# Kernel tuning notes

Hardware: AMD Instinct MI355X
Metric: run time of the kernel (lower is better)

The kernel has to match this reference:

```python
import jax, jax.numpy as jnp
import numpy as np

INPUT_DIM = 128
NUM_CLASSES = 10
MAX_DEPTH = 8
HID = 16            # effective_transform_output_dim
TEMP = 1.0
EFF_IN = INPUT_DIM + 2          # root features + parent score + grandparent score
N_INTERNAL = 2 ** MAX_DEPTH - 1  # 255, level-order stacked
N_LEAVES = 2 ** MAX_DEPTH        # 256
BATCH = 32768


def setup_inputs() -> dict:
    key = jax.random.key(0)
    ks = jax.random.split(key, 6)
    x = jax.random.normal(ks[0], (BATCH, INPUT_DIM), jnp.float32)
    path_prob = jnp.ones((BATCH, 1), jnp.float32)
    W1 = jax.random.normal(ks[1], (N_INTERNAL, EFF_IN, HID), jnp.float32) * (1.0 / np.sqrt(EFF_IN))
    b1 = jax.random.normal(ks[2], (N_INTERNAL, HID), jnp.float32) * 0.01
    w2 = jax.random.normal(ks[3], (N_INTERNAL, HID), jnp.float32) * (1.0 / np.sqrt(HID))
    b2 = jax.random.normal(ks[4], (N_INTERNAL,), jnp.float32) * 0.01
    leaf_logits = jax.random.normal(ks[5], (N_LEAVES, NUM_CLASSES), jnp.float32)
    return {"x": x, "path_prob": path_prob, "W1": W1, "b1": b1,
            "w2": w2, "b2": b2, "leaf_logits": leaf_logits}


def reference(x, path_prob, W1, b1, w2, b2, leaf_logits):
    """Depth-batched soft binary tree: all 2^d nodes at depth d are processed
    as one batched GEMM instead of the original sequential recursion."""
    B = x.shape[0]
    pp = path_prob                              # [B, n_nodes_at_depth]
    parent = jnp.zeros((B, 1), x.dtype)         # parent decision scores (0 => unused at depth 0)
    grandp = jnp.zeros((B, 1), x.dtype)         # grandparent scores (0 => unused at depth 0,1)
    for d in range(MAX_DEPTH):
        lo, hi = 2 ** d - 1, 2 ** (d + 1) - 1   # level-order slice of this depth's nodes
        W1d = W1[lo:hi]                          # [N, EFF_IN, HID]
        # concat([x, parent, grandparent]) @ W1d without materializing the concat
        h = jnp.einsum('be,neh->bnh', x, W1d[:, :INPUT_DIM, :])
        h = h + parent[:, :, None] * W1d[None, :, INPUT_DIM, :]
        h = h + grandp[:, :, None] * W1d[None, :, INPUT_DIM + 1, :]
        t = jax.nn.relu(h + b1[lo:hi][None])                       # [B, N, HID]
        score = jnp.einsum('bnh,nh->bn', t, w2[lo:hi]) + b2[lo:hi][None]  # [B, N]
        p = jax.nn.sigmoid(score / TEMP)
        n = pp.shape[1]
        # children: left gets p, right gets 1-p; level-order interleave
        pp = jnp.stack([pp * p, pp * (1.0 - p)], axis=-1).reshape(B, 2 * n)
        grandp = jnp.repeat(parent, 2, axis=1)   # child's grandparent = node's parent
        parent = jnp.repeat(score, 2, axis=1)    # child's parent_out = this node's raw score
    # leaves: sum_n path_prob[:, n] * output_logits[n]
    return jnp.einsum('bn,nc->bc', pp, leaf_logits)
```

## Files before the change

kernel.cpp:

```cpp
#include <hip/hip_runtime.h>
#include <math.h>

namespace {

typedef __attribute__((ext_vector_type(8))) __fp16 f16x8;
typedef __attribute__((ext_vector_type(4))) float f32x4;

constexpr int IN_DIM = 128;
constexpr int EFF    = 130 * 16;
constexpr int NODES  = 255;
constexpr int TS     = 64;
constexpr int BLOCK  = 256;
constexpr int NC     = 10;

__global__ __launch_bounds__(256) void prep_w1(const float* __restrict__ W1,
                                               f16x8* __restrict__ wfrag) {
    __shared__ float xs[IN_DIM * 16];
    const int n = blockIdx.x, tid = threadIdx.x;
    const float4* src = (const float4*)(W1 + (size_t)n * EFF);
    ((float4*)xs)[tid]       = src[tid];
    ((float4*)xs)[tid + 256] = src[tid + 256];
    __syncthreads();
    const int l = tid & 63, t = tid >> 6;
    const int k0 = t * 32 + (l >> 4) * 8, hid = l & 15;
    f16x8 hv;
    #pragma unroll
    for (int j = 0; j < 8; ++j)
        hv[j] = (__fp16)xs[(k0 + j) * 16 + hid];
    wfrag[(n * 4 + t) * 64 + l] = hv;
}

__device__ __forceinline__ void loadW(const f16x8* __restrict__ wfrag, int n, int l,
                                      f16x8 (&w)[4]) {
    const f16x8* wp = wfrag + (size_t)n * 256 + l;
    #pragma unroll
    for (int t = 0; t < 4; ++t) w[t] = wp[t * 64];
}

__device__ __forceinline__ void mfma16(const f16x8 (&w)[4], const f16x8 (&xh)[4][4],
                                       f32x4 (&acc)[4]) {
    #pragma unroll
    for (int t = 0; t < 4; ++t)
        #pragma unroll
        for (int mt = 0; mt < 4; ++mt)
            acc[mt] = __builtin_amdgcn_mfma_f32_16x16x32_f16(w[t], xh[t][mt], acc[mt], 0, 0, 0);
}

__device__ __forceinline__ float epilogue_score(
    const f32x4 (&acc)[4], const float4& w2q, const float4& wpq, const float4& wgq,
    const float (&par)[4], const float (&gp)[4], float b2v, int quad)
{
    float score01[4];
    #pragma unroll
    for (int mt = 0; mt < 4; ++mt) {
        float ts = 0.0f;
        #pragma unroll
        for (int r = 0; r < 4; ++r) {
            const float wpr = (r == 0) ? wpq.x : (r == 1) ? wpq.y : (r == 2) ? wpq.z : wpq.w;
            const float wgr = (r == 0) ? wgq.x : (r == 1) ? wgq.y : (r == 2) ? wgq.z : wgq.w;
            const float w2r = (r == 0) ? w2q.x : (r == 1) ? w2q.y : (r == 2) ? w2q.z : w2q.w;
            const float h = fmaf(par[mt], wpr, fmaf(gp[mt], wgr, acc[mt][r]));
            ts = fmaf(fmaxf(h, 0.0f), w2r, ts);
        }
        ts += __shfl_xor(ts, 16);
        ts += __shfl_xor(ts, 32);
        score01[mt] = ts;
    }
    const float sa = (quad & 1) ? score01[1] : score01[0];
    const float sb = (quad & 1) ? score01[3] : score01[2];
    return ((quad & 2) ? sb : sa) + b2v;
}

__global__ __launch_bounds__(BLOCK) __attribute__((amdgpu_waves_per_eu(2, 2)))
void tree_mfma(
    const float* __restrict__ x, const float* __restrict__ path_prob,
    const float* __restrict__ W1, const float* __restrict__ b1,
    const float* __restrict__ w2, const float* __restrict__ b2,
    const float* __restrict__ leaf_logits,
    const f16x8* __restrict__ wfrag,
    float* __restrict__ out)
{
    __shared__ float pp[128][TS];
    __shared__ float scbuf[127][TS];

    const int tid  = threadIdx.x;
    const int wv   = tid >> 6, l = tid & 63;
    const int quad = l >> 4,   col = l & 15;
    const int s0   = blockIdx.x * TS;

    if (tid < TS) pp[0][tid] = path_prob[s0 + tid];

    f16x8 xh[4][4];
    #pragma unroll
    for (int t = 0; t < 4; ++t)
        #pragma unroll
        for (int mt = 0; mt < 4; ++mt) {
            const float* xp = x + (size_t)(s0 + mt * 16 + col) * IN_DIM + t * 32 + quad * 8;
            float4 v0 = ((const float4*)xp)[0];
            float4 v1 = ((const float4*)xp)[1];
            float vv[8] = {v0.x, v0.y, v0.z, v0.w, v1.x, v1.y, v1.z, v1.w};
            f16x8 hv;
            #pragma unroll
            for (int j = 0; j < 8; ++j) hv[j] = (__fp16)vv[j];
            xh[t][mt] = hv;
        }

    for (int d = 0; d < 7; ++d) {
        const int nd = 1 << d;
        float (*scW)[TS]  = (float(*)[TS])&scbuf[nd - 1][0];
        float (*scP)[TS]  = (float(*)[TS])&scbuf[(nd >> 1) - 1][0];
        float (*scP2)[TS] = (float(*)[TS])&scbuf[(nd >> 2) - 1][0];
        const int stride = 128 >> d, half = 64 >> d;

        int nlo, nhi;
        if (d >= 2) { nlo = wv * (nd >> 2); nhi = nlo + (nd >> 2); }
        else        { nlo = wv; nhi = (wv < nd) ? wv + 1 : wv; }

        bool havePrev = false;
        f32x4 accP[4];
        float4 p_w2q, p_wpq, p_wgq;
        float  p_b2v = 0.f, p_ppar = 0.f;
        float  p_par[4], p_gp[4];
        int    p_slot = 0, p_nl = 0;

        for (int nl = nlo; nl < nhi; ++nl) {
            const int n = nd - 1 + nl;

            f16x8 w[4];
            loadW(wfrag, n, l, w);
            const float4 b1q = ((const float4*)(b1 + n * 16))[quad];

            if (havePrev) {
                const float sv = epilogue_score(accP, p_w2q, p_wpq, p_wgq, p_par, p_gp, p_b2v, quad);
                scW[p_nl][l] = sv;
                const float p = 1.0f / (1.0f + __expf(-sv));
                pp[p_slot][l]        = p_ppar * p;
                pp[p_slot + half][l] = p_ppar * (1.0f - p);
            }

            const float4 w2q = ((const float4*)(w2 + n * 16))[quad];
            const float4 wpq = ((const float4*)(W1 + (size_t)n * EFF + 128 * 16))[quad];
            const float4 wgq = ((const float4*)(W1 + (size_t)n * EFF + 129 * 16))[quad];
            const float  b2v = b2[n];
            const int    slot = nl * stride;
            const float  ppar = pp[slot][l];
            float par[4], gp[4];
            #pragma unroll
            for (int mt = 0; mt < 4; ++mt) {
                const int scol = mt * 16 + col;
                par[mt] = (d >= 1) ? scP[nl >> 1][scol] : 0.0f;
                gp[mt]  = (d >= 2) ? scP2[nl >> 2][scol] : 0.0f;
            }

            f32x4 binit = {b1q.x, b1q.y, b1q.z, b1q.w};
            f32x4 acc[4] = {binit, binit, binit, binit};
            mfma16(w, xh, acc);

            #pragma unroll
            for (int mt = 0; mt < 4; ++mt) accP[mt] = acc[mt];
            p_w2q = w2q; p_wpq = wpq; p_wgq = wgq;
            p_b2v = b2v; p_ppar = ppar;
            #pragma unroll
            for (int mt = 0; mt < 4; ++mt) { p_par[mt] = par[mt]; p_gp[mt] = gp[mt]; }
            p_slot = slot; p_nl = nl;
            havePrev = true;
        }
        if (havePrev) {
            const float sv = epilogue_score(accP, p_w2q, p_wpq, p_wgq, p_par, p_gp, p_b2v, quad);
            scW[p_nl][l] = sv;
            const float p = 1.0f / (1.0f + __expf(-sv));
            pp[p_slot][l]        = p_ppar * p;
            pp[p_slot + half][l] = p_ppar * (1.0f - p);
        }
        if (d < 2) __syncthreads();
    }

    float oacc[NC];
    #pragma unroll
    for (int c = 0; c < NC; ++c) oacc[c] = 0.0f;
    {
        float (*scP)[TS]  = (float(*)[TS])&scbuf[63][0];
        float (*scP2)[TS] = (float(*)[TS])&scbuf[31][0];

        bool havePrev = false;
        f32x4 accP[4];
        float4 p_w2q, p_wpq, p_wgq;
        float  p_b2v = 0.f, p_ppar = 0.f;
        float  p_par[4], p_gp[4];
        int    p_nl = 0;

        const int nlo = wv * 32, nhi = nlo + 32;
        for (int nl = nlo; nl < nhi; ++nl) {
            const int n = 127 + nl;

            f16x8 w[4];
            loadW(wfrag, n, l, w);
            const float4 b1q = ((const float4*)(b1 + n * 16))[quad];

            if (havePrev) {
                const float sv = epilogue_score(accP, p_w2q, p_wpq, p_wgq, p_par, p_gp, p_b2v, quad);
                const float p = 1.0f / (1.0f + __expf(-sv));
                const float pL = p_ppar * p;
                const float pR = p_ppar * (1.0f - p);
                const float* llp = leaf_logits + (size_t)(2 * p_nl) * NC;
                #pragma unroll
                for (int c = 0; c < NC; ++c)
                    oacc[c] = fmaf(pL, llp[c], fmaf(pR, llp[NC + c], oacc[c]));
            }

            const float4 w2q = ((const float4*)(w2 + n * 16))[quad];
            const float4 wpq = ((const float4*)(W1 + (size_t)n * EFF + 128 * 16))[quad];
            const float4 wgq = ((const float4*)(W1 + (size_t)n * EFF + 129 * 16))[quad];
            const float  b2v = b2[n];
            const float  ppar = pp[nl][l];
            float par[4], gp[4];
            #pragma unroll
            for (int mt = 0; mt < 4; ++mt) {
                const int scol = mt * 16 + col;
                par[mt] = scP[nl >> 1][scol];
                gp[mt]  = scP2[nl >> 2][scol];
            }

            f32x4 binit = {b1q.x, b1q.y, b1q.z, b1q.w};
            f32x4 acc[4] = {binit, binit, binit, binit};
            mfma16(w, xh, acc);

            #pragma unroll
            for (int mt = 0; mt < 4; ++mt) accP[mt] = acc[mt];
            p_w2q = w2q; p_wpq = wpq; p_wgq = wgq;
            p_b2v = b2v; p_ppar = ppar;
            #pragma unroll
            for (int mt = 0; mt < 4; ++mt) { p_par[mt] = par[mt]; p_gp[mt] = gp[mt]; }
            p_nl = nl;
            havePrev = true;
        }
        if (havePrev) {
            const float sv = epilogue_score(accP, p_w2q, p_wpq, p_wgq, p_par, p_gp, p_b2v, quad);
            const float p = 1.0f / (1.0f + __expf(-sv));
            const float pL = p_ppar * p;
            const float pR = p_ppar * (1.0f - p);
            const float* llp = leaf_logits + (size_t)(2 * p_nl) * NC;
            #pragma unroll
            for (int c = 0; c < NC; ++c)
                oacc[c] = fmaf(pL, llp[c], fmaf(pR, llp[NC + c], oacc[c]));
        }
    }

    __syncthreads();
    {
        float* red = &scbuf[0][0];
        #pragma unroll
        for (int c = 0; c < NC; ++c)
            red[(wv * 64 + l) * NC + c] = oacc[c];
    }
    __syncthreads();
    {
        const float* red = &scbuf[0][0];
        for (int i = tid; i < TS * NC; i += BLOCK) {
            float v = red[i] + red[640 + i] + red[1280 + i] + red[1920 + i];
            out[(size_t)s0 * NC + i] = v;
        }
    }
}

}

extern "C" void kernel_launch(void* const* d_in, const int* in_sizes, int n_in,
                              void* d_out, int out_size, void* d_ws, size_t ws_size,
                              hipStream_t stream) {
    const float* x           = (const float*)d_in[0];
    const float* path_prob   = (const float*)d_in[1];
    const float* W1          = (const float*)d_in[2];
    const float* b1          = (const float*)d_in[3];
    const float* w2          = (const float*)d_in[4];
    const float* b2          = (const float*)d_in[5];
    const float* leaf_logits = (const float*)d_in[6];
    float* out = (float*)d_out;

    const int batch = in_sizes[0] / IN_DIM;
    f16x8* wfrag = (f16x8*)d_ws;

    hipLaunchKernelGGL(prep_w1, dim3(NODES), dim3(256), 0, stream, W1, wfrag);
    hipLaunchKernelGGL(tree_mfma, dim3(batch / TS), dim3(BLOCK), 0, stream,
                       x, path_prob, W1, b1, w2, b2, leaf_logits, wfrag, out);
}
```

Measured before the change: 137.5 us.

## Halve sample tile and process node pairs per wave to double block count

Shrinks the per-block sample tile from 64 to 32 rows, which doubles the grid size, and restructures each wave to compute two tree nodes at once. The two nodes share the x fragments, and the lane quads split their epilogue outputs between nodes. The waves_per_eu cap is relaxed to allow more occupancy, and the final reduction is reindexed for the new lane-to-sample mapping. The change aims at more parallelism and less per-wave register pressure. In exchange, every block reloads the full weight set, so total weight traffic doubles, and depths 0-2 now leave lanes idle.

```diff
diff --git a/kernel.cpp b/kernel.cpp
--- a/kernel.cpp
+++ b/kernel.cpp
@@ -9,7 +9,7 @@
 constexpr int IN_DIM = 128;
 constexpr int EFF    = 130 * 16;
 constexpr int NODES  = 255;
-constexpr int TS     = 64;
+constexpr int TS     = 32;
 constexpr int BLOCK  = 256;
 constexpr int NC     = 10;
 
@@ -37,41 +37,59 @@
     for (int t = 0; t < 4; ++t) w[t] = wp[t * 64];
 }
 
-__device__ __forceinline__ void mfma16(const f16x8 (&w)[4], const f16x8 (&xh)[4][4],
-                                       f32x4 (&acc)[4]) {
-    #pragma unroll
-    for (int t = 0; t < 4; ++t)
-        #pragma unroll
-        for (int mt = 0; mt < 4; ++mt)
-            acc[mt] = __builtin_amdgcn_mfma_f32_16x16x32_f16(w[t], xh[t][mt], acc[mt], 0, 0, 0);
-}
-
-__device__ __forceinline__ float epilogue_score(
-    const f32x4 (&acc)[4], const float4& w2q, const float4& wpq, const float4& wgq,
-    const float (&par)[4], const float (&gp)[4], float b2v, int quad)
+#define COMP4(v, r) ((r == 0) ? v.x : (r == 1) ? v.y : (r == 2) ? v.z : v.w)
+
+__device__ __forceinline__ float epi_pair(
+    const f32x4 (&accA)[2], const f32x4 (&accB)[2],
+    const float4& w2A, const float4& w2B,
+    const float4& wpA, const float4& wpB,
+    const float4& wgA, const float4& wgB,
+    const float (&par)[2], const float (&gp)[2],
+    float b2A, float b2B, int quad)
 {
-    float score01[4];
-    #pragma unroll
-    for (int mt = 0; mt < 4; ++mt) {
-        float ts = 0.0f;
-        #pragma unroll
-        for (int r = 0; r < 4; ++r) {
-            const float wpr = (r == 0) ? wpq.x : (r == 1) ? wpq.y : (r == 2) ? wpq.z : wpq.w;
-            const float wgr = (r == 0) ? wgq.x : (r == 1) ? wgq.y : (r == 2) ? wgq.z : wgq.w;
-            const float w2r = (r == 0) ? w2q.x : (r == 1) ? w2q.y : (r == 2) ? w2q.z : w2q.w;
-            const float h = fmaf(par[mt], wpr, fmaf(gp[mt], wgr, acc[mt][r]));
-            ts = fmaf(fmaxf(h, 0.0f), w2r, ts);
-        }
-        ts += __shfl_xor(ts, 16);
-        ts += __shfl_xor(ts, 32);
-        score01[mt] = ts;
-    }
-    const float sa = (quad & 1) ? score01[1] : score01[0];
-    const float sb = (quad & 1) ? score01[3] : score01[2];
-    return ((quad & 2) ? sb : sa) + b2v;
-}
-
-__global__ __launch_bounds__(BLOCK) __attribute__((amdgpu_waves_per_eu(2, 2)))
+    float sc0 = 0.f, sc1 = 0.f, sc2 = 0.f, sc3 = 0.f;
+    #pragma unroll
+    for (int r = 0; r < 4; ++r) {
+        const float wpAr = COMP4(wpA, r), wpBr = COMP4(wpB, r);
+        const float wgAr = COMP4(wgA, r), wgBr = COMP4(wgB, r);
+        const float w2Ar = COMP4(w2A, r), w2Br = COMP4(w2B, r);
+        const float hA0 = fmaf(par[0], wpAr, fmaf(gp[0], wgAr, accA[0][r]));
+        const float hA1 = fmaf(par[1], wpAr, fmaf(gp[1], wgAr, accA[1][r]));
+        const float hB0 = fmaf(par[0], wpBr, fmaf(gp[0], wgBr, accB[0][r]));
+        const float hB1 = fmaf(par[1], wpBr, fmaf(gp[1], wgBr, accB[1][r]));
+        sc0 = fmaf(fmaxf(hA0, 0.0f), w2Ar, sc0);
+        sc1 = fmaf(fmaxf(hA1, 0.0f), w2Ar, sc1);
+        sc2 = fmaf(fmaxf(hB0, 0.0f), w2Br, sc2);
+        sc3 = fmaf(fmaxf(hB1, 0.0f), w2Br, sc3);
+    }
+    sc0 += __shfl_xor(sc0, 16); sc0 += __shfl_xor(sc0, 32);
+    sc1 += __shfl_xor(sc1, 16); sc1 += __shfl_xor(sc1, 32);
+    sc2 += __shfl_xor(sc2, 16); sc2 += __shfl_xor(sc2, 32);
+    sc3 += __shfl_xor(sc3, 16); sc3 += __shfl_xor(sc3, 32);
+    const float sa = (quad & 1) ? sc1 : sc0;
+    const float sb = (quad & 1) ? sc3 : sc2;
+    return ((quad & 2) ? sb : sa) + ((quad & 2) ? b2B : b2A);
+}
+
+__device__ __forceinline__ float epi_single(
+    const f32x4 (&acc)[2], const float4& w2q, const float4& wpq, const float4& wgq,
+    const float (&par)[2], const float (&gp)[2], float b2v, int quad)
+{
+    float sc0 = 0.f, sc1 = 0.f;
+    #pragma unroll
+    for (int r = 0; r < 4; ++r) {
+        const float wpr = COMP4(wpq, r), wgr = COMP4(wgq, r), w2r = COMP4(w2q, r);
+        const float h0 = fmaf(par[0], wpr, fmaf(gp[0], wgr, acc[0][r]));
+        const float h1 = fmaf(par[1], wpr, fmaf(gp[1], wgr, acc[1][r]));
+        sc0 = fmaf(fmaxf(h0, 0.0f), w2r, sc0);
+        sc1 = fmaf(fmaxf(h1, 0.0f), w2r, sc1);
+    }
+    sc0 += __shfl_xor(sc0, 16); sc0 += __shfl_xor(sc0, 32);
+    sc1 += __shfl_xor(sc1, 16); sc1 += __shfl_xor(sc1, 32);
+    return ((quad & 1) ? sc1 : sc0) + b2v;
+}
+
+__global__ __launch_bounds__(BLOCK) __attribute__((amdgpu_waves_per_eu(2)))
 void tree_mfma(
     const float* __restrict__ x, const float* __restrict__ path_prob,
     const float* __restrict__ W1, const float* __restrict__ b1,
@@ -86,15 +104,17 @@
     const int tid  = threadIdx.x;
     const int wv   = tid >> 6, l = tid & 63;
     const int quad = l >> 4,   col = l & 15;
+    const int sl   = l & 31;
+    const int nodeIdx = quad >> 1;
     const int s0   = blockIdx.x * TS;
 
     if (tid < TS) pp[0][tid] = path_prob[s0 + tid];
 
-    f16x8 xh[4][4];
+    f16x8 xh[4][2];
     #pragma unroll
     for (int t = 0; t < 4; ++t)
         #pragma unroll
-        for (int mt = 0; mt < 4; ++mt) {
+        for (int mt = 0; mt < 2; ++mt) {
             const float* xp = x + (size_t)(s0 + mt * 16 + col) * IN_DIM + t * 32 + quad * 8;
             float4 v0 = ((const float4*)xp)[0];
             float4 v1 = ((const float4*)xp)[1];
@@ -105,141 +125,198 @@
             xh[t][mt] = hv;
         }
 
-    for (int d = 0; d < 7; ++d) {
+    for (int d = 0; d < 3; ++d) {
         const int nd = 1 << d;
-        float (*scW)[TS]  = (float(*)[TS])&scbuf[nd - 1][0];
-        float (*scP)[TS]  = (float(*)[TS])&scbuf[(nd >> 1) - 1][0];
-        float (*scP2)[TS] = (float(*)[TS])&scbuf[(nd >> 2) - 1][0];
         const int stride = 128 >> d, half = 64 >> d;
-
-        int nlo, nhi;
-        if (d >= 2) { nlo = wv * (nd >> 2); nhi = nlo + (nd >> 2); }
-        else        { nlo = wv; nhi = (wv < nd) ? wv + 1 : wv; }
-
-        bool havePrev = false;
-        f32x4 accP[4];
-        float4 p_w2q, p_wpq, p_wgq;
-        float  p_b2v = 0.f, p_ppar = 0.f;
-        float  p_par[4], p_gp[4];
-        int    p_slot = 0, p_nl = 0;
-
-        for (int nl = nlo; nl < nhi; ++nl) {
-            const int n = nd - 1 + nl;
-
+        if (wv < nd) {
+            const int n = nd - 1 + wv;
             f16x8 w[4];
             loadW(wfrag, n, l, w);
             const float4 b1q = ((const float4*)(b1 + n * 16))[quad];
-
-            if (havePrev) {
-                const float sv = epilogue_score(accP, p_w2q, p_wpq, p_wgq, p_par, p_gp, p_b2v, quad);
-                scW[p_nl][l] = sv;
-                const float p = 1.0f / (1.0f + __expf(-sv));
-                pp[p_slot][l]        = p_ppar * p;
-                pp[p_slot + half][l] = p_ppar * (1.0f - p);
-            }
-
             const float4 w2q = ((const float4*)(w2 + n * 16))[quad];
             const float4 wpq = ((const float4*)(W1 + (size_t)n * EFF + 128 * 16))[quad];
             const float4 wgq = ((const float4*)(W1 + (size_t)n * EFF + 129 * 16))[quad];
             const float  b2v = b2[n];
-            const int    slot = nl * stride;
-            const float  ppar = pp[slot][l];
-            float par[4], gp[4];
-            #pragma unroll
-            for (int mt = 0; mt < 4; ++mt) {
+            float par[2], gp[2];
+            #pragma unroll
+            for (int mt = 0; mt < 2; ++mt) {
                 const int scol = mt * 16 + col;
-                par[mt] = (d >= 1) ? scP[nl >> 1][scol] : 0.0f;
-                gp[mt]  = (d >= 2) ? scP2[nl >> 2][scol] : 0.0f;
-            }
+                par[mt] = (d >= 1) ? scbuf[(nd >> 1) - 1 + (wv >> 1)][scol] : 0.0f;
+                gp[mt]  = (d >= 2) ? scbuf[(nd >> 2) - 1 + (wv >> 2)][scol] : 0.0f;
+            }
+            const int   slot = wv * stride;
+            const float ppar = pp[slot][sl];
 
             f32x4 binit = {b1q.x, b1q.y, b1q.z, b1q.w};
-            f32x4 acc[4] = {binit, binit, binit, binit};
-            mfma16(w, xh, acc);
-
-            #pragma unroll
-            for (int mt = 0; mt < 4; ++mt) accP[mt] = acc[mt];
-            p_w2q = w2q; p_wpq = wpq; p_wgq = wgq;
-            p_b2v = b2v; p_ppar = ppar;
-            #pragma unroll
-            for (int mt = 0; mt < 4; ++mt) { p_par[mt] = par[mt]; p_gp[mt] = gp[mt]; }
-            p_slot = slot; p_nl = nl;
+            f32x4 acc[2] = {binit, binit};
+            #pragma unroll
+            for (int t = 0; t < 4; ++t) {
+                acc[0] = __builtin_amdgcn_mfma_f32_16x16x32_f16(w[t], xh[t][0], acc[0], 0, 0, 0);
+                acc[1] = __builtin_amdgcn_mfma_f32_16x16x32_f16(w[t], xh[t][1], acc[1], 0, 0, 0);
+            }
+            const float sv = epi_single(acc, w2q, wpq, wgq, par, gp, b2v, quad);
+            if (l < 32) {
+                scbuf[nd - 1 + wv][sl] = sv;
+                const float p = 1.0f / (1.0f + __expf(-sv));
+                pp[slot][sl]        = ppar * p;
+                pp[slot + half][sl] = ppar * (1.0f - p);
+            }
+        }
+        if (d < 2) __syncthreads();
+    }
+
+    bool havePrev = false;
+    f32x4  pAccA[2], pAccB[2];
+    float4 pW2A, pW2B, pWpA, pWpB, pWgA, pWgB;
+    float  pB2A = 0.f, pB2B = 0.f, pPpar = 0.f;
+    float  pPar[2], pGp[2];
+    int    pScwAbs = 0, pSlotBase = 0, pStride = 0, pHalf = 0;
+
+    for (int d = 3; d < 7; ++d) {
+        const int nd = 1 << d;
+        const int stride = 128 >> d, half = 64 >> d;
+        const int scWo = nd - 1, scPo = (nd >> 1) - 1, scP2o = (nd >> 2) - 1;
+        const int plo = wv * (nd >> 3), phi = plo + (nd >> 3);
+        for (int pl = plo; pl < phi; ++pl) {
+            const int nA = nd - 1 + 2 * pl, nB = nA + 1;
+
+            f16x8 wA[4], wB[4];
+            loadW(wfrag, nA, l, wA);
+            loadW(wfrag, nB, l, wB);
+            const float4 b1A = ((const float4*)(b1 + nA * 16))[quad];
+            const float4 b1B = ((const float4*)(b1 + nB * 16))[quad];
+
+            if (havePrev) {
+                const float sv = epi_pair(pAccA, pAccB, pW2A, pW2B, pWpA, pWpB,
+                                          pWgA, pWgB, pPar, pGp, pB2A, pB2B, quad);
+                scbuf[pScwAbs + nodeIdx][sl] = sv;
+                const float p = 1.0f / (1.0f + __expf(-sv));
+                const int slot = pSlotBase + nodeIdx * pStride;
+                pp[slot][sl]         = pPpar * p;
+                pp[slot + pHalf][sl] = pPpar * (1.0f - p);
+            }
+
+            const float4 w2A = ((const float4*)(w2 + nA * 16))[quad];
+            const float4 w2B = ((const float4*)(w2 + nB * 16))[quad];
+            const float4 wpA = ((const float4*)(W1 + (size_t)nA * EFF + 128 * 16))[quad];
+            const float4 wpB = ((const float4*)(W1 + (size_t)nB * EFF + 128 * 16))[quad];
+            const float4 wgA = ((const float4*)(W1 + (size_t)nA * EFF + 129 * 16))[quad];
+            const float4 wgB = ((const float4*)(W1 + (size_t)nB * EFF + 129 * 16))[quad];
+            const float  b2A = b2[nA], b2B = b2[nB];
+            float par[2], gp[2];
+            #pragma unroll
+            for (int mt = 0; mt < 2; ++mt) {
+                const int scol = mt * 16 + col;
+                par[mt] = scbuf[scPo + pl][scol];
+                gp[mt]  = scbuf[scP2o + (pl >> 1)][scol];
+            }
+            const float ppar = pp[(2 * pl + nodeIdx) * stride][sl];
+
+            f32x4 binitA = {b1A.x, b1A.y, b1A.z, b1A.w};
+            f32x4 binitB = {b1B.x, b1B.y, b1B.z, b1B.w};
+            f32x4 accA[2] = {binitA, binitA};
+            f32x4 accB[2] = {binitB, binitB};
+            #pragma unroll
+            for (int t = 0; t < 4; ++t) {
+                accA[0] = __builtin_amdgcn_mfma_f32_16x16x32_f16(wA[t], xh[t][0], accA[0], 0, 0, 0);
+                accA[1] = __builtin_amdgcn_mfma_f32_16x16x32_f16(wA[t], xh[t][1], accA[1], 0, 0, 0);
+                accB[0] = __builtin_amdgcn_mfma_f32_16x16x32_f16(wB[t], xh[t][0], accB[0], 0, 0, 0);
+                accB[1] = __builtin_amdgcn_mfma_f32_16x16x32_f16(wB[t], xh[t][1], accB[1], 0, 0, 0);
+            }
+
+            pAccA[0] = accA[0]; pAccA[1] = accA[1];
+            pAccB[0] = accB[0]; pAccB[1] = accB[1];
+            pW2A = w2A; pW2B = w2B; pWpA = wpA; pWpB = wpB; pWgA = wgA; pWgB = wgB;
+            pB2A = b2A; pB2B = b2B; pPpar = ppar;
+            pPar[0] = par[0]; pPar[1] = par[1]; pGp[0] = gp[0]; pGp[1] = gp[1];
+            pScwAbs = scWo + 2 * pl; pSlotBase = 2 * pl * stride;
+            pStride = stride; pHalf = half;
             havePrev = true;
         }
-        if (havePrev) {
-            const float sv = epilogue_score(accP, p_w2q, p_wpq, p_wgq, p_par, p_gp, p_b2v, quad);
-            scW[p_nl][l] = sv;
-            const float p = 1.0f / (1.0f + __expf(-sv));
-            pp[p_slot][l]        = p_ppar * p;
-            pp[p_slot + half][l] = p_ppar * (1.0f - p);
-        }
-        if (d < 2) __syncthreads();
+    }
+    if (havePrev) {
+        const float sv = epi_pair(pAccA, pAccB, pW2A, pW2B, pWpA, pWpB,
+                                  pWgA, pWgB, pPar, pGp, pB2A, pB2B, quad);
+        scbuf[pScwAbs + nodeIdx][sl] = sv;
+        const float p = 1.0f / (1.0f + __expf(-sv));
+        const int slot = pSlotBase + nodeIdx * pStride;
+        pp[slot][sl]         = pPpar * p;
+        pp[slot + pHalf][sl] = pPpar * (1.0f - p);
     }
 
     float oacc[NC];
     #pragma unroll
     for (int c = 0; c < NC; ++c) oacc[c] = 0.0f;
     {
-        float (*scP)[TS]  = (float(*)[TS])&scbuf[63][0];
-        float (*scP2)[TS] = (float(*)[TS])&scbuf[31][0];
-
-        bool havePrev = false;
-        f32x4 accP[4];
-        float4 p_w2q, p_wpq, p_wgq;
-        float  p_b2v = 0.f, p_ppar = 0.f;
-        float  p_par[4], p_gp[4];
-        int    p_nl = 0;
-
-        const int nlo = wv * 32, nhi = nlo + 32;
-        for (int nl = nlo; nl < nhi; ++nl) {
-            const int n = 127 + nl;
-
-            f16x8 w[4];
-            loadW(wfrag, n, l, w);
-            const float4 b1q = ((const float4*)(b1 + n * 16))[quad];
-
-            if (havePrev) {
-                const float sv = epilogue_score(accP, p_w2q, p_wpq, p_wgq, p_par, p_gp, p_b2v, quad);
-                const float p = 1.0f / (1.0f + __expf(-sv));
-                const float pL = p_ppar * p;
-                const float pR = p_ppar * (1.0f - p);
-                const float* llp = leaf_logits + (size_t)(2 * p_nl) * NC;
+        bool hp = false;
+        int  pPl = 0;
+        const int plo = wv * 16, phi = plo + 16;
+        for (int pl = plo; pl < phi; ++pl) {
+            const int nA = 127 + 2 * pl, nB = nA + 1;
+
+            f16x8 wA[4], wB[4];
+            loadW(wfrag, nA, l, wA);
+            loadW(wfrag, nB, l, wB);
+            const float4 b1A = ((const float4*)(b1 + nA * 16))[quad];
+            const float4 b1B = ((const float4*)(b1 + nB * 16))[quad];
+
+            if (hp) {
+                const float sv = epi_pair(pAccA, pAccB, pW2A, pW2B, pWpA, pWpB,
+                                          pWgA, pWgB, pPar, pGp, pB2A, pB2B, quad);
+                const float p  = 1.0f / (1.0f + __expf(-sv));
+                const float pL = pPpar * p;
+                const float pR = pPpar * (1.0f - p);
+                const int   nid = 2 * pPl + nodeIdx;
+                const float* llp = leaf_logits + (size_t)(2 * nid) * NC;
                 #pragma unroll
                 for (int c = 0; c < NC; ++c)
                     oacc[c] = fmaf(pL, llp[c], fmaf(pR, llp[NC + c], oacc[c]));
             }
 
-            const float4 w2q = ((const float4*)(w2 + n * 16))[quad];
-            const float4 wpq = ((const float4*)(W1 + (size_t)n * EFF + 128 * 16))[quad];
-            const float4 wgq = ((const float4*)(W1 + (size_t)n * EFF + 129 * 16))[quad];
-            const float  b2v = b2[n];
-            const float  ppar = pp[nl][l];
-            float par[4], gp[4];
-            #pragma unroll
-            for (int mt = 0; mt < 4; ++mt) {
+            const float4 w2A = ((const float4*)(w2 + nA * 16))[quad];
+            const float4 w2B = ((const float4*)(w2 + nB * 16))[quad];
+            const float4 wpA = ((const float4*)(W1 + (size_t)nA * EFF + 128 * 16))[quad];
+            const float4 wpB = ((const float4*)(W1 + (size_t)nB * EFF + 128 * 16))[quad];
+            const float4 wgA = ((const float4*)(W1 + (size_t)nA * EFF + 129 * 16))[quad];
+            const float4 wgB = ((const float4*)(W1 + (size_t)nB * EFF + 129 * 16))[quad];
+            const float  b2A = b2[nA], b2B = b2[nB];
+            float par[2], gp[2];
+            #pragma unroll
+            for (int mt = 0; mt < 2; ++mt) {
                 const int scol = mt * 16 + col;
-                par[mt] = scP[nl >> 1][scol];
-                gp[mt]  = scP2[nl >> 2][scol];
-            }
-
-            f32x4 binit = {b1q.x, b1q.y, b1q.z, b1q.w};
-            f32x4 acc[4] = {binit, binit, binit, binit};
-            mfma16(w, xh, acc);
-
-            #pragma unroll
-            for (int mt = 0; mt < 4; ++mt) accP[mt] = acc[mt];
-            p_w2q = w2q; p_wpq = wpq; p_wgq = wgq;
-            p_b2v = b2v; p_ppar = ppar;
-            #pragma unroll
-            for (int mt = 0; mt < 4; ++mt) { p_par[mt] = par[mt]; p_gp[mt] = gp[mt]; }
-            p_nl = nl;
-            havePrev = true;
-        }
-        if (havePrev) {
-            const float sv = epilogue_score(accP, p_w2q, p_wpq, p_wgq, p_par, p_gp, p_b2v, quad);
-            const float p = 1.0f / (1.0f + __expf(-sv));
-            const float pL = p_ppar * p;
-            const float pR = p_ppar * (1.0f - p);
-            const float* llp = leaf_logits + (size_t)(2 * p_nl) * NC;
+                par[mt] = scbuf[63 + pl][scol];
+                gp[mt]  = scbuf[31 + (pl >> 1)][scol];
+            }
+            const float ppar = pp[2 * pl + nodeIdx][sl];
+
+            f32x4 binitA = {b1A.x, b1A.y, b1A.z, b1A.w};
+            f32x4 binitB = {b1B.x, b1B.y, b1B.z, b1B.w};
+            f32x4 accA[2] = {binitA, binitA};
+            f32x4 accB[2] = {binitB, binitB};
+            #pragma unroll
+            for (int t = 0; t < 4; ++t) {
+                accA[0] = __builtin_amdgcn_mfma_f32_16x16x32_f16(wA[t], xh[t][0], accA[0], 0, 0, 0);
+                accA[1] = __builtin_amdgcn_mfma_f32_16x16x32_f16(wA[t], xh[t][1], accA[1], 0, 0, 0);
+                accB[0] = __builtin_amdgcn_mfma_f32_16x16x32_f16(wB[t], xh[t][0], accB[0], 0, 0, 0);
+                accB[1] = __builtin_amdgcn_mfma_f32_16x16x32_f16(wB[t], xh[t][1], accB[1], 0, 0, 0);
+            }
+
+            pAccA[0] = accA[0]; pAccA[1] = accA[1];
+            pAccB[0] = accB[0]; pAccB[1] = accB[1];
+            pW2A = w2A; pW2B = w2B; pWpA = wpA; pWpB = wpB; pWgA = wgA; pWgB = wgB;
+            pB2A = b2A; pB2B = b2B; pPpar = ppar;
+            pPar[0] = par[0]; pPar[1] = par[1]; pGp[0] = gp[0]; pGp[1] = gp[1];
+            pPl = pl;
+            hp = true;
+        }
+        if (hp) {
+            const float sv = epi_pair(pAccA, pAccB, pW2A, pW2B, pWpA, pWpB,
+                                      pWgA, pWgB, pPar, pGp, pB2A, pB2B, quad);
+            const float p  = 1.0f / (1.0f + __expf(-sv));
+            const float pL = pPpar * p;
+            const float pR = pPpar * (1.0f - p);
+            const int   nid = 2 * pPl + nodeIdx;
+            const float* llp = leaf_logits + (size_t)(2 * nid) * NC;
             #pragma unroll
             for (int c = 0; c < NC; ++c)
                 oacc[c] = fmaf(pL, llp[c], fmaf(pR, llp[NC + c], oacc[c]));
@@ -257,7 +334,11 @@
     {
         const float* red = &scbuf[0][0];
         for (int i = tid; i < TS * NC; i += BLOCK) {
-            float v = red[i] + red[640 + i] + red[1280 + i] + red[1920 + i];
+            const int s = i / NC, c = i - s * NC;
+            float v = 0.0f;
+            #pragma unroll
+            for (int w = 0; w < 4; ++w)
+                v += red[(w * 64 + s) * NC + c] + red[(w * 64 + 32 + s) * NC + c];
             out[(size_t)s0 * NC + i] = v;
         }
     }
```

New measurement: 160.4 us. 1.17x slower.

## Process sibling node pairs per iteration and cut epilogue shuffle count

Applied to the files above, without the earlier changes.

Replaces the software-pipelined one-node-per-iteration loops with loops that handle two sibling nodes at a time, sharing parent/grandparent score loads and interleaving two independent MFMA chains so they hide each other's latency. The epilogue reduction is rewritten to exchange partial sums with three shuffles instead of eight per node. Leaf logits are loaded as wide float4 vectors, the first three depths are fully unrolled, and the waves-per-EU cap is relaxed. The trade-off is higher register pressure from two accumulator sets, which may reduce occupancy or cause spills.

```diff
diff --git a/kernel.cpp b/kernel.cpp
--- a/kernel.cpp
+++ b/kernel.cpp
@@ -46,32 +46,40 @@
             acc[mt] = __builtin_amdgcn_mfma_f32_16x16x32_f16(w[t], xh[t][mt], acc[mt], 0, 0, 0);
 }
 
-__device__ __forceinline__ float epilogue_score(
+#define COMP4(v, r) ((r == 0) ? v.x : (r == 1) ? v.y : (r == 2) ? v.z : v.w)
+
+__device__ __forceinline__ float epi_score(
     const f32x4 (&acc)[4], const float4& w2q, const float4& wpq, const float4& wgq,
     const float (&par)[4], const float (&gp)[4], float b2v, int quad)
 {
-    float score01[4];
+    float p4[4];
     #pragma unroll
     for (int mt = 0; mt < 4; ++mt) {
         float ts = 0.0f;
         #pragma unroll
         for (int r = 0; r < 4; ++r) {
-            const float wpr = (r == 0) ? wpq.x : (r == 1) ? wpq.y : (r == 2) ? wpq.z : wpq.w;
-            const float wgr = (r == 0) ? wgq.x : (r == 1) ? wgq.y : (r == 2) ? wgq.z : wgq.w;
-            const float w2r = (r == 0) ? w2q.x : (r == 1) ? w2q.y : (r == 2) ? w2q.z : w2q.w;
+            const float wpr = COMP4(wpq, r);
+            const float wgr = COMP4(wgq, r);
+            const float w2r = COMP4(w2q, r);
             const float h = fmaf(par[mt], wpr, fmaf(gp[mt], wgr, acc[mt][r]));
             ts = fmaf(fmaxf(h, 0.0f), w2r, ts);
         }
-        ts += __shfl_xor(ts, 16);
-        ts += __shfl_xor(ts, 32);
-        score01[mt] = ts;
-    }
-    const float sa = (quad & 1) ? score01[1] : score01[0];
-    const float sb = (quad & 1) ? score01[3] : score01[2];
-    return ((quad & 2) ? sb : sa) + b2v;
-}
-
-__global__ __launch_bounds__(BLOCK) __attribute__((amdgpu_waves_per_eu(2, 2)))
+        p4[mt] = ts;
+    }
+    const bool hiQ = (quad & 2) != 0;
+    const bool loQ = (quad & 1) != 0;
+    const float a  = hiQ ? p4[2] : p4[0];
+    const float b  = hiQ ? p4[3] : p4[1];
+    const float sa = hiQ ? p4[0] : p4[2];
+    const float sb = hiQ ? p4[1] : p4[3];
+    const float uA = a + __shfl_xor(sa, 32);
+    const float uB = b + __shfl_xor(sb, 32);
+    const float k  = loQ ? uB : uA;
+    const float s  = loQ ? uA : uB;
+    return k + __shfl_xor(s, 16) + b2v;
+}
+
+__global__ __launch_bounds__(BLOCK) __attribute__((amdgpu_waves_per_eu(2)))
 void tree_mfma(
     const float* __restrict__ x, const float* __restrict__ path_prob,
     const float* __restrict__ W1, const float* __restrict__ b1,
@@ -105,144 +113,146 @@
             xh[t][mt] = hv;
         }
 
-    for (int d = 0; d < 7; ++d) {
+    #pragma unroll
+    for (int d = 0; d < 3; ++d) {
         const int nd = 1 << d;
-        float (*scW)[TS]  = (float(*)[TS])&scbuf[nd - 1][0];
-        float (*scP)[TS]  = (float(*)[TS])&scbuf[(nd >> 1) - 1][0];
-        float (*scP2)[TS] = (float(*)[TS])&scbuf[(nd >> 2) - 1][0];
         const int stride = 128 >> d, half = 64 >> d;
-
-        int nlo, nhi;
-        if (d >= 2) { nlo = wv * (nd >> 2); nhi = nlo + (nd >> 2); }
-        else        { nlo = wv; nhi = (wv < nd) ? wv + 1 : wv; }
-
-        bool havePrev = false;
-        f32x4 accP[4];
-        float4 p_w2q, p_wpq, p_wgq;
-        float  p_b2v = 0.f, p_ppar = 0.f;
-        float  p_par[4], p_gp[4];
-        int    p_slot = 0, p_nl = 0;
-
-        for (int nl = nlo; nl < nhi; ++nl) {
-            const int n = nd - 1 + nl;
-
+        if (wv < nd) {
+            const int n = nd - 1 + wv;
             f16x8 w[4];
             loadW(wfrag, n, l, w);
             const float4 b1q = ((const float4*)(b1 + n * 16))[quad];
-
-            if (havePrev) {
-                const float sv = epilogue_score(accP, p_w2q, p_wpq, p_wgq, p_par, p_gp, p_b2v, quad);
-                scW[p_nl][l] = sv;
-                const float p = 1.0f / (1.0f + __expf(-sv));
-                pp[p_slot][l]        = p_ppar * p;
-                pp[p_slot + half][l] = p_ppar * (1.0f - p);
-            }
-
             const float4 w2q = ((const float4*)(w2 + n * 16))[quad];
             const float4 wpq = ((const float4*)(W1 + (size_t)n * EFF + 128 * 16))[quad];
             const float4 wgq = ((const float4*)(W1 + (size_t)n * EFF + 129 * 16))[quad];
             const float  b2v = b2[n];
-            const int    slot = nl * stride;
-            const float  ppar = pp[slot][l];
             float par[4], gp[4];
             #pragma unroll
             for (int mt = 0; mt < 4; ++mt) {
                 const int scol = mt * 16 + col;
-                par[mt] = (d >= 1) ? scP[nl >> 1][scol] : 0.0f;
-                gp[mt]  = (d >= 2) ? scP2[nl >> 2][scol] : 0.0f;
+                par[mt] = (d >= 1) ? scbuf[(nd >> 1) - 1 + (wv >> 1)][scol] : 0.0f;
+                gp[mt]  = (d >= 2) ? scbuf[(nd >> 2) - 1 + (wv >> 2)][scol] : 0.0f;
             }
+            const int   slot = wv * stride;
+            const float ppar = pp[slot][l];
 
             f32x4 binit = {b1q.x, b1q.y, b1q.z, b1q.w};
             f32x4 acc[4] = {binit, binit, binit, binit};
             mfma16(w, xh, acc);
 
-            #pragma unroll
-            for (int mt = 0; mt < 4; ++mt) accP[mt] = acc[mt];
-            p_w2q = w2q; p_wpq = wpq; p_wgq = wgq;
-            p_b2v = b2v; p_ppar = ppar;
-            #pragma unroll
-            for (int mt = 0; mt < 4; ++mt) { p_par[mt] = par[mt]; p_gp[mt] = gp[mt]; }
-            p_slot = slot; p_nl = nl;
-            havePrev = true;
-        }
-        if (havePrev) {
-            const float sv = epilogue_score(accP, p_w2q, p_wpq, p_wgq, p_par, p_gp, p_b2v, quad);
-            scW[p_nl][l] = sv;
+            const float sv = epi_score(acc, w2q, wpq, wgq, par, gp, b2v, quad);
+            scbuf[nd - 1 + wv][l] = sv;
             const float p = 1.0f / (1.0f + __expf(-sv));
-            pp[p_slot][l]        = p_ppar * p;
-            pp[p_slot + half][l] = p_ppar * (1.0f - p);
+            pp[slot][l]        = ppar * p;
+            pp[slot + half][l] = ppar * (1.0f - p);
         }
         if (d < 2) __syncthreads();
+    }
+
+    for (int d = 3; d < 7; ++d) {
+        const int nd = 1 << d;
+        const int stride = 128 >> d, half = 64 >> d;
+        const int base = nd - 1, scPo = (nd >> 1) - 1, scP2o = (nd >> 2) - 1;
+        const int ilo = wv * (nd >> 3), ihi = ilo + (nd >> 3);
+        for (int i = ilo; i < ihi; ++i) {
+            const int nA = base + 2 * i, nB = nA + 1;
+
+            f16x8 wA[4], wB[4];
+            loadW(wfrag, nA, l, wA);
+            loadW(wfrag, nB, l, wB);
+            const float4 b1A = ((const float4*)(b1 + nA * 16))[quad];
+            const float4 b1B = ((const float4*)(b1 + nB * 16))[quad];
+            const float4 w2A = ((const float4*)(w2 + nA * 16))[quad];
+            const float4 w2B = ((const float4*)(w2 + nB * 16))[quad];
+            const float4 wpA = ((const float4*)(W1 + (size_t)nA * EFF + 128 * 16))[quad];
+            const float4 wpB = ((const float4*)(W1 + (size_t)nB * EFF + 128 * 16))[quad];
+            const float4 wgA = ((const float4*)(W1 + (size_t)nA * EFF + 129 * 16))[quad];
+            const float4 wgB = ((const float4*)(W1 + (size_t)nB * EFF + 129 * 16))[quad];
+            const float  b2A = b2[nA], b2B = b2[nB];
+            float par[4], gp[4];
+            #pragma unroll
+            for (int mt = 0; mt < 4; ++mt) {
+                const int scol = mt * 16 + col;
+                par[mt] = scbuf[scPo + i][scol];
+                gp[mt]  = scbuf[scP2o + (i >> 1)][scol];
+            }
+            const int   slotA = (2 * i) * stride, slotB = slotA + stride;
+            const float pparA = pp[slotA][l], pparB = pp[slotB][l];
+
+            f32x4 iAi = {b1A.x, b1A.y, b1A.z, b1A.w};
+            f32x4 iBi = {b1B.x, b1B.y, b1B.z, b1B.w};
+            f32x4 accA[4] = {iAi, iAi, iAi, iAi};
+            f32x4 accB[4] = {iBi, iBi, iBi, iBi};
+            mfma16(wA, xh, accA);
+            mfma16(wB, xh, accB);
+
+            const float svA = epi_score(accA, w2A, wpA, wgA, par, gp, b2A, quad);
+            const float svB = epi_score(accB, w2B, wpB, wgB, par, gp, b2B, quad);
+            scbuf[base + 2 * i][l]     = svA;
+            scbuf[base + 2 * i + 1][l] = svB;
+            const float pA = 1.0f / (1.0f + __expf(-svA));
+            const float pB = 1.0f / (1.0f + __expf(-svB));
+            pp[slotA][l]        = pparA * pA;
+            pp[slotA + half][l] = pparA * (1.0f - pA);
+            pp[slotB][l]        = pparB * pB;
+            pp[slotB + half][l] = pparB * (1.0f - pB);
+        }
     }
 
     float oacc[NC];
     #pragma unroll
     for (int c = 0; c < NC; ++c) oacc[c] = 0.0f;
     {
-        float (*scP)[TS]  = (float(*)[TS])&scbuf[63][0];
-        float (*scP2)[TS] = (float(*)[TS])&scbuf[31][0];
-
-        bool havePrev = false;
-        f32x4 accP[4];
-        float4 p_w2q, p_wpq, p_wgq;
-        float  p_b2v = 0.f, p_ppar = 0.f;
-        float  p_par[4], p_gp[4];
-        int    p_nl = 0;
-
-        const int nlo = wv * 32, nhi = nlo + 32;
-        for (int nl = nlo; nl < nhi; ++nl) {
-            const int n = 127 + nl;
-
-            f16x8 w[4];
-            loadW(wfrag, n, l, w);
-            const float4 b1q = ((const float4*)(b1 + n * 16))[quad];
-
-            if (havePrev) {
-                const float sv = epilogue_score(accP, p_w2q, p_wpq, p_wgq, p_par, p_gp, p_b2v, quad);
-                const float p = 1.0f / (1.0f + __expf(-sv));
-                const float pL = p_ppar * p;
-                const float pR = p_ppar * (1.0f - p);
-                const float* llp = leaf_logits + (size_t)(2 * p_nl) * NC;
-                #pragma unroll
-                for (int c = 0; c < NC; ++c)
-                    oacc[c] = fmaf(pL, llp[c], fmaf(pR, llp[NC + c], oacc[c]));
-            }
-
-            const float4 w2q = ((const float4*)(w2 + n * 16))[quad];
-            const float4 wpq = ((const float4*)(W1 + (size_t)n * EFF + 128 * 16))[quad];
-            const float4 wgq = ((const float4*)(W1 + (size_t)n * EFF + 129 * 16))[quad];
-            const float  b2v = b2[n];
-            const float  ppar = pp[nl][l];
+        const int ilo = wv * 16, ihi = ilo + 16;
+        for (int i = ilo; i < ihi; ++i) {
+            const int nA = 127 + 2 * i, nB = nA + 1;
+
+            f16x8 wA[4], wB[4];
+            loadW(wfrag, nA, l, wA);
+            loadW(wfrag, nB, l, wB);
+            const float4 b1A = ((const float4*)(b1 + nA * 16))[quad];
+            const float4 b1B = ((const float4*)(b1 + nB * 16))[quad];
+            const float4 w2A = ((const float4*)(w2 + nA * 16))[quad];
+            const float4 w2B = ((const float4*)(w2 + nB * 16))[quad];
+            const float4 wpA = ((const float4*)(W1 + (size_t)nA * EFF + 128 * 16))[quad];
+            const float4 wpB = ((const float4*)(W1 + (size_t)nB * EFF + 128 * 16))[quad];
+            const float4 wgA = ((const float4*)(W1 + (size_t)nA * EFF + 129 * 16))[quad];
+            const float4 wgB = ((const float4*)(W1 + (size_t)nB * EFF + 129 * 16))[quad];
+            const float  b2A = b2[nA], b2B = b2[nB];
             float par[4], gp[4];
             #pragma unroll
             for (int mt = 0; mt < 4; ++mt) {
                 const int scol = mt * 16 + col;
-                par[mt] = scP[nl >> 1][scol];
-                gp[mt]  = scP2[nl >> 2][scol];
+                par[mt] = scbuf[63 + i][scol];
+                gp[mt]  = scbuf[31 + (i >> 1)][scol];
             }
-
-            f32x4 binit = {b1q.x, b1q.y, b1q.z, b1q.w};
-            f32x4 acc[4] = {binit, binit, binit, binit};
-            mfma16(w, xh, acc);
-
-            #pragma unroll
-            for (int mt = 0; mt < 4; ++mt) accP[mt] = acc[mt];
-            p_w2q = w2q; p_wpq = wpq; p_wgq = wgq;
-            p_b2v = b2v; p_ppar = ppar;
-            #pragma unroll
-            for (int mt = 0; mt < 4; ++mt) { p_par[mt] = par[mt]; p_gp[mt] = gp[mt]; }
-            p_nl = nl;
-            havePrev = true;
-        }
-        if (havePrev) {
-            const float sv = epilogue_score(accP, p_w2q, p_wpq, p_wgq, p_par, p_gp, p_b2v, quad);
-            const float p = 1.0f / (1.0f + __expf(-sv));
-            const float pL = p_ppar * p;
-            const float pR = p_ppar * (1.0f - p);
-            const float* llp = leaf_logits + (size_t)(2 * p_nl) * NC;
+            const float pparA = pp[2 * i][l], pparB = pp[2 * i + 1][l];
+
+            f32x4 iAi = {b1A.x, b1A.y, b1A.z, b1A.w};
+            f32x4 iBi = {b1B.x, b1B.y, b1B.z, b1B.w};
+            f32x4 accA[4] = {iAi, iAi, iAi, iAi};
+            f32x4 accB[4] = {iBi, iBi, iBi, iBi};
+            mfma16(wA, xh, accA);
+            mfma16(wB, xh, accB);
+
+            const float4* lp4 = (const float4*)(leaf_logits + (size_t)(4 * i) * NC);
+            float4 lv[10];
+            #pragma unroll
+            for (int q = 0; q < 10; ++q) lv[q] = lp4[q];
+            const float* lf = (const float*)lv;
+
+            const float svA = epi_score(accA, w2A, wpA, wgA, par, gp, b2A, quad);
+            const float svB = epi_score(accB, w2B, wpB, wgB, par, gp, b2B, quad);
+            const float pA = 1.0f / (1.0f + __expf(-svA));
+            const float pB = 1.0f / (1.0f + __expf(-svB));
+            const float pLA = pparA * pA, pRA = pparA * (1.0f - pA);
+            const float pLB = pparB * pB, pRB = pparB * (1.0f - pB);
             #pragma unroll
             for (int c = 0; c < NC; ++c)
-                oacc[c] = fmaf(pL, llp[c], fmaf(pR, llp[NC + c], oacc[c]));
+                oacc[c] = fmaf(pLA, lf[c], fmaf(pRA, lf[NC + c], oacc[c]));
+            #pragma unroll
+            for (int c = 0; c < NC; ++c)
+                oacc[c] = fmaf(pLB, lf[2 * NC + c], fmaf(pRB, lf[3 * NC + c], oacc[c]));
         }
     }
 
```

Measured after the change: 142.1 us. +3.4%, slower.
